# Performance work log

Hardware: AMD Instinct MI355X
Metric: run time of the kernel (lower is better)

## Reference

```python
import jax, jax.numpy as jnp
import numpy as np


def setup_inputs() -> dict:
    key = jax.random.key(0)
    k1, k2, k3, k4, k5 = jax.random.split(key, 5)
    C, Cr = 512, 64  # in_channels, in_channels // 8
    B, W, H = 16, 64, 64
    x = jax.random.normal(k1, (B, C, W, H), dtype=jnp.float32)
    # 1x1 conv == pointwise linear over channels; store as [out, in]
    w1 = jax.random.normal(k2, (Cr, C), dtype=jnp.float32) * (1.0 / np.sqrt(C))
    b1 = jax.random.normal(k3, (Cr,), dtype=jnp.float32) * 0.01
    w2 = jax.random.normal(k4, (C, Cr), dtype=jnp.float32) * (1.0 / np.sqrt(Cr))
    b2 = jax.random.normal(k5, (C,), dtype=jnp.float32) * 0.01
    return {"x": x, "w1": w1, "b1": b1, "w2": w2, "b2": b2}


def reference(x, w1, b1, w2, b2):
    B, C, W, H = x.shape
    # conv1x1: channel reduction C -> C//8
    r = jnp.einsum('bchw,oc->bohw', x, w1) + b1[None, :, None, None]
    q = r.reshape(B, -1, W * H)                      # [B, C', N] query/key/value
    # channel-channel attention map [B, C', C'] (bmm(query, key^T))
    att = jnp.einsum('bcn,bdn->bcd', q, q)
    att = jax.nn.softmax(att, axis=-1)
    out = jnp.einsum('bcd,bdn->bcn', att, q)          # [B, C', N]
    out = out.reshape(B, -1, W, H)
    # conv_out: channel expansion C//8 -> C, plus residual
    out = jnp.einsum('bchw,oc->bohw', out, w2) + b2[None, :, None, None]
    return out + x
```

## Files before the change

kernel.cpp:

```cpp
#include <hip/hip_runtime.h>
#include <math.h>

#define NPIX 4096
#define CIN  512
#define CR   64
#define NB   16

typedef __bf16 bf16x8 __attribute__((ext_vector_type(8)));
typedef float  f32x4  __attribute__((ext_vector_type(4)));
typedef unsigned int uint;
typedef uint   uint4v __attribute__((ext_vector_type(4)));
typedef unsigned short ushort;

static const size_t W1B_OFF = 0;
static const size_t Q_OFF   = W1B_OFF + 65536;
static const size_t QT_OFF  = Q_OFF  + (size_t)NB*CR*NPIX*2;
static const size_t ATT_OFF = QT_OFF + (size_t)NB*NPIX*CR*2;
static const size_t MB_OFF  = ATT_OFF + (size_t)NB*CR*CR*4;

static __device__ inline uint pk_bf16(float a, float b) {
    uint r;
    asm volatile("v_cvt_pk_bf16_f32 %0, %1, %2" : "=v"(r) : "v"(a), "v"(b));
    return r;
}

__global__ __launch_bounds__(256) void k0_cast(const float* __restrict__ w1,
                                               uint* __restrict__ w1b) {
    int i = blockIdx.x * 256 + threadIdx.x;
    w1b[i] = pk_bf16(w1[2 * i], w1[2 * i + 1]);
}

__global__ __launch_bounds__(256) void k1_conv1(const float* __restrict__ x,
                                                const ushort* __restrict__ w1b,
                                                const float* __restrict__ b1,
                                                ushort* __restrict__ q,
                                                ushort* __restrict__ qt) {
    int b = blockIdx.y;
    int t = threadIdx.x;
    int wid = t >> 6, l = t & 63;
    int lo = l & 15, kg = l >> 4;
    int px0 = blockIdx.x * 256 + wid * 64;
    const float* xb = x + (size_t)b * CIN * NPIX;

    f32x4 acc[4][4] = {};
    for (int ks = 0; ks < 16; ks++) {
        int k0 = ks * 32 + kg * 8;
        float xv[4][8];
#pragma unroll
        for (int pf = 0; pf < 4; pf++) {
            const float* xp = xb + (size_t)k0 * NPIX + px0 + pf * 16 + lo;
#pragma unroll
            for (int j = 0; j < 8; j++) xv[pf][j] = xp[(size_t)j * NPIX];
        }
        bf16x8 af[4];
#pragma unroll
        for (int of = 0; of < 4; of++)
            af[of] = *(const bf16x8*)(w1b + (size_t)(of * 16 + lo) * CIN + k0);
#pragma unroll
        for (int pf = 0; pf < 4; pf++) {
            uint4v bu;
#pragma unroll
            for (int j = 0; j < 4; j++) bu[j] = pk_bf16(xv[pf][2 * j], xv[pf][2 * j + 1]);
            bf16x8 bf = __builtin_bit_cast(bf16x8, bu);
#pragma unroll
            for (int of = 0; of < 4; of++)
                acc[pf][of] = __builtin_amdgcn_mfma_f32_16x16x32_bf16(af[of], bf, acc[pf][of], 0, 0, 0);
        }
    }
#pragma unroll
    for (int pf = 0; pf < 4; pf++) {
        int px = px0 + pf * 16 + lo;
        ushort* qb  = q  + (size_t)b * CR * NPIX + px;
        ushort* qtb = qt + ((size_t)b * NPIX + px) * CR;
#pragma unroll
        for (int of = 0; of < 4; of++) {
            int o = of * 16 + kg * 4;
            float v0 = acc[pf][of][0] + b1[o + 0];
            float v1 = acc[pf][of][1] + b1[o + 1];
            float v2 = acc[pf][of][2] + b1[o + 2];
            float v3 = acc[pf][of][3] + b1[o + 3];
            uint p0 = pk_bf16(v0, v1), p1 = pk_bf16(v2, v3);
            qb[(size_t)(o + 0) * NPIX] = (ushort)(p0 & 0xffff);
            qb[(size_t)(o + 1) * NPIX] = (ushort)(p0 >> 16);
            qb[(size_t)(o + 2) * NPIX] = (ushort)(p1 & 0xffff);
            qb[(size_t)(o + 3) * NPIX] = (ushort)(p1 >> 16);
            *(uint2*)(qtb + o) = make_uint2(p0, p1);
        }
    }
}

__global__ __launch_bounds__(512) void k2_att(const ushort* __restrict__ q,
                                              float* __restrict__ att) {
    __shared__ float part[8][64][66];
    int b = blockIdx.x;
    int t = threadIdx.x;
    int w = t >> 6, l = t & 63;
    int lo = l & 15, kg = l >> 4;
    const ushort* qb = q + (size_t)b * CR * NPIX + w * 512;

    f32x4 acc[4][4] = {};
    for (int ks = 0; ks < 16; ks++) {
        bf16x8 fr[4];
#pragma unroll
        for (int cf = 0; cf < 4; cf++)
            fr[cf] = *(const bf16x8*)(qb + (size_t)(cf * 16 + lo) * NPIX + ks * 32 + kg * 8);
#pragma unroll
        for (int cf = 0; cf < 4; cf++)
#pragma unroll
            for (int df = 0; df < 4; df++)
                acc[cf][df] = __builtin_amdgcn_mfma_f32_16x16x32_bf16(fr[cf], fr[df], acc[cf][df], 0, 0, 0);
    }
#pragma unroll
    for (int cf = 0; cf < 4; cf++)
#pragma unroll
        for (int df = 0; df < 4; df++)
#pragma unroll
            for (int r = 0; r < 4; r++)
                part[w][cf * 16 + kg * 4 + r][df * 16 + lo] = acc[cf][df][r];
    __syncthreads();

#pragma unroll
    for (int i = 0; i < 8; i++) {
        int c = w * 8 + i;
        float v = 0.f;
#pragma unroll
        for (int pw = 0; pw < 8; pw++) v += part[pw][c][l];
        float m = v;
#pragma unroll
        for (int s = 1; s < 64; s <<= 1) m = fmaxf(m, __shfl_xor(m, s, 64));
        float e = __expf(v - m);
        float ssum = e;
#pragma unroll
        for (int s = 1; s < 64; s <<= 1) ssum += __shfl_xor(ssum, s, 64);
        att[((size_t)b * CR + c) * CR + l] = e / ssum;
    }
}

__global__ __launch_bounds__(256) void k3_m(const float* __restrict__ w2,
                                            const float* __restrict__ att,
                                            ushort* __restrict__ mb) {
    int b = blockIdx.y;
    int c  = (blockIdx.x >> 2) * 256 + threadIdx.x;
    int dg = (blockIdx.x & 3) * 16;
    const float* ab  = att + (size_t)b * CR * CR + dg;
    const float* w2r = w2 + (size_t)c * CR;
    float acc[16];
#pragma unroll
    for (int j = 0; j < 16; j++) acc[j] = 0.f;
    for (int k = 0; k < CR; k++) {
        float wv = w2r[k];
#pragma unroll
        for (int j4 = 0; j4 < 4; j4++) {
            f32x4 av = *(const f32x4*)(ab + k * CR + j4 * 4);
#pragma unroll
            for (int u = 0; u < 4; u++)
                acc[j4 * 4 + u] = fmaf(wv, av[u], acc[j4 * 4 + u]);
        }
    }
    uint* mp = (uint*)(mb + ((size_t)b * CIN + c) * CR + dg);
#pragma unroll
    for (int i = 0; i < 8; i++)
        mp[i] = pk_bf16(acc[2 * i], acc[2 * i + 1]);
}

__global__ __launch_bounds__(256) void k4_out(const ushort* __restrict__ qt,
                                              const ushort* __restrict__ mb,
                                              const float* __restrict__ b2,
                                              const float* __restrict__ x,
                                              float* __restrict__ y) {
    int cc = blockIdx.x, b = blockIdx.z;
    int t = threadIdx.x;
    int wid = t >> 6, l = t & 63;
    int lo = l & 15, kg = l >> 4;
    int px0 = blockIdx.y * 128 + wid * 32;
    int pxA = px0 + lo, pxB = px0 + 16 + lo;
    const ushort* qpA = qt + ((size_t)b * NPIX + pxA) * CR;
    const ushort* qpB = qt + ((size_t)b * NPIX + pxB) * CR;
    const ushort* mp = mb + ((size_t)b * CIN + cc * 64) * CR;

    bf16x8 bqA0 = *(const bf16x8*)(qpA + kg * 8);
    bf16x8 bqA1 = *(const bf16x8*)(qpA + 32 + kg * 8);
    bf16x8 bqB0 = *(const bf16x8*)(qpB + kg * 8);
    bf16x8 bqB1 = *(const bf16x8*)(qpB + 32 + kg * 8);
    bf16x8 am[4][2];
#pragma unroll
    for (int cf = 0; cf < 4; cf++) {
        am[cf][0] = *(const bf16x8*)(mp + (size_t)(cf * 16 + lo) * CR + kg * 8);
        am[cf][1] = *(const bf16x8*)(mp + (size_t)(cf * 16 + lo) * CR + 32 + kg * 8);
    }
    float xrA[4][4], xrB[4][4];
#pragma unroll
    for (int cf = 0; cf < 4; cf++)
#pragma unroll
        for (int r = 0; r < 4; r++) {
            size_t row = ((size_t)b * CIN + cc * 64 + cf * 16 + kg * 4 + r) * NPIX;
            xrA[cf][r] = x[row + pxA];
            xrB[cf][r] = x[row + pxB];
        }

    f32x4 accA[4] = {}, accB[4] = {};
#pragma unroll
    for (int cf = 0; cf < 4; cf++) {
        accA[cf] = __builtin_amdgcn_mfma_f32_16x16x32_bf16(am[cf][0], bqA0, accA[cf], 0, 0, 0);
        accA[cf] = __builtin_amdgcn_mfma_f32_16x16x32_bf16(am[cf][1], bqA1, accA[cf], 0, 0, 0);
        accB[cf] = __builtin_amdgcn_mfma_f32_16x16x32_bf16(am[cf][0], bqB0, accB[cf], 0, 0, 0);
        accB[cf] = __builtin_amdgcn_mfma_f32_16x16x32_bf16(am[cf][1], bqB1, accB[cf], 0, 0, 0);
    }
#pragma unroll
    for (int cf = 0; cf < 4; cf++) {
        int c = cc * 64 + cf * 16 + kg * 4;
#pragma unroll
        for (int r = 0; r < 4; r++) {
            size_t row = ((size_t)b * CIN + c + r) * NPIX;
            y[row + pxA] = accA[cf][r] + b2[c + r] + xrA[cf][r];
            y[row + pxB] = accB[cf][r] + b2[c + r] + xrB[cf][r];
        }
    }
}

extern "C" void kernel_launch(void* const* d_in, const int* in_sizes, int n_in,
                              void* d_out, int out_size, void* d_ws, size_t ws_size,
                              hipStream_t stream) {
    const float* x  = (const float*)d_in[0];
    const float* w1 = (const float*)d_in[1];
    const float* b1 = (const float*)d_in[2];
    const float* w2 = (const float*)d_in[3];
    const float* b2 = (const float*)d_in[4];
    float* y = (float*)d_out;
    char* ws = (char*)d_ws;

    uint*   w1b = (uint*)  (ws + W1B_OFF);
    ushort* q   = (ushort*)(ws + Q_OFF);
    ushort* qt  = (ushort*)(ws + QT_OFF);
    float*  att = (float*) (ws + ATT_OFF);
    ushort* mb  = (ushort*)(ws + MB_OFF);

    hipLaunchKernelGGL(k0_cast,  dim3(64),         dim3(256), 0, stream, w1, w1b);
    hipLaunchKernelGGL(k1_conv1, dim3(16, 16),     dim3(256), 0, stream, x, (const ushort*)w1b, b1, q, qt);
    hipLaunchKernelGGL(k2_att,   dim3(16),         dim3(512), 0, stream, q, att);
    hipLaunchKernelGGL(k3_m,     dim3(8, 16),      dim3(256), 0, stream, w2, att, mb);
    hipLaunchKernelGGL(k4_out,   dim3(8, 32, 16),  dim3(256), 0, stream, qt, mb, b2, x, y);
}
```

Measured before the change: 118.5 us.

## Double-buffer conv1 loads, tile qt for coalesced stores, widen att block

The conv1 kernel now double-buffers its x and weight loads across K-steps, so global loads for the next step are issued while MFMAs run on the current one. The transposed q buffer is re-laid out in MFMA-fragment-tiled order, making both the conv1 stores and the output-kernel loads contiguous across lanes. The attention kernel uses 1024 threads (16 waves), each reducing half as many pixels, with a two-phase shared-memory accumulation. The cost is higher register pressure in conv1 and an extra sync in the attention kernel.

```diff
diff --git a/kernel.cpp b/kernel.cpp
--- a/kernel.cpp
+++ b/kernel.cpp
@@ -18,6 +18,7 @@
 static const size_t ATT_OFF = QT_OFF + (size_t)NB*NPIX*CR*2;
 static const size_t MB_OFF  = ATT_OFF + (size_t)NB*CR*CR*4;
 
+
 static __device__ inline uint pk_bf16(float a, float b) {
     uint r;
     asm volatile("v_cvt_pk_bf16_f32 %0, %1, %2" : "=v"(r) : "v"(a), "v"(b));
@@ -30,48 +31,64 @@
     w1b[i] = pk_bf16(w1[2 * i], w1[2 * i + 1]);
 }
 
+#define K1_LOAD(XV, AF, KS) do {                                             \
+    int k0_ = (KS) * 32 + kg * 8;                                            \
+    _Pragma("unroll")                                                        \
+    for (int pf = 0; pf < 4; pf++) {                                         \
+        const float* xp_ = xb + (size_t)k0_ * NPIX + pf * 16;                \
+        _Pragma("unroll")                                                    \
+        for (int j = 0; j < 8; j++) XV[pf][j] = xp_[(size_t)j * NPIX];       \
+    }                                                                        \
+    _Pragma("unroll")                                                        \
+    for (int of = 0; of < 4; of++)                                           \
+        AF[of] = *(const bf16x8*)(w1b + (size_t)(of * 16 + lo) * CIN + k0_); \
+} while (0)
+
+#define K1_COMPUTE(XV, AF) do {                                              \
+    _Pragma("unroll")                                                        \
+    for (int pf = 0; pf < 4; pf++) {                                         \
+        uint4v bu_;                                                          \
+        _Pragma("unroll")                                                    \
+        for (int j = 0; j < 4; j++)                                          \
+            bu_[j] = pk_bf16(XV[pf][2 * j], XV[pf][2 * j + 1]);              \
+        bf16x8 bf_ = __builtin_bit_cast(bf16x8, bu_);                        \
+        _Pragma("unroll")                                                    \
+        for (int of = 0; of < 4; of++)                                       \
+            acc[pf][of] = __builtin_amdgcn_mfma_f32_16x16x32_bf16(           \
+                AF[of], bf_, acc[pf][of], 0, 0, 0);                          \
+    }                                                                        \
+} while (0)
+
 __global__ __launch_bounds__(256) void k1_conv1(const float* __restrict__ x,
                                                 const ushort* __restrict__ w1b,
                                                 const float* __restrict__ b1,
                                                 ushort* __restrict__ q,
-                                                ushort* __restrict__ qt) {
+                                                uint2* __restrict__ qt4) {
     int b = blockIdx.y;
     int t = threadIdx.x;
     int wid = t >> 6, l = t & 63;
     int lo = l & 15, kg = l >> 4;
     int px0 = blockIdx.x * 256 + wid * 64;
-    const float* xb = x + (size_t)b * CIN * NPIX;
+    const float* xb = x + (size_t)b * CIN * NPIX + px0 + lo;
 
     f32x4 acc[4][4] = {};
-    for (int ks = 0; ks < 16; ks++) {
-        int k0 = ks * 32 + kg * 8;
-        float xv[4][8];
-#pragma unroll
-        for (int pf = 0; pf < 4; pf++) {
-            const float* xp = xb + (size_t)k0 * NPIX + px0 + pf * 16 + lo;
-#pragma unroll
-            for (int j = 0; j < 8; j++) xv[pf][j] = xp[(size_t)j * NPIX];
-        }
-        bf16x8 af[4];
-#pragma unroll
-        for (int of = 0; of < 4; of++)
-            af[of] = *(const bf16x8*)(w1b + (size_t)(of * 16 + lo) * CIN + k0);
-#pragma unroll
-        for (int pf = 0; pf < 4; pf++) {
-            uint4v bu;
-#pragma unroll
-            for (int j = 0; j < 4; j++) bu[j] = pk_bf16(xv[pf][2 * j], xv[pf][2 * j + 1]);
-            bf16x8 bf = __builtin_bit_cast(bf16x8, bu);
-#pragma unroll
-            for (int of = 0; of < 4; of++)
-                acc[pf][of] = __builtin_amdgcn_mfma_f32_16x16x32_bf16(af[of], bf, acc[pf][of], 0, 0, 0);
-        }
-    }
+    float xvA[4][8], xvB[4][8];
+    bf16x8 afA[4], afB[4];
+
+    K1_LOAD(xvA, afA, 0);
+#pragma unroll
+    for (int ks2 = 0; ks2 < 8; ks2++) {
+        K1_LOAD(xvB, afB, 2 * ks2 + 1);
+        K1_COMPUTE(xvA, afA);
+        if (ks2 < 7) K1_LOAD(xvA, afA, 2 * ks2 + 2);
+        K1_COMPUTE(xvB, afB);
+    }
+
 #pragma unroll
     for (int pf = 0; pf < 4; pf++) {
         int px = px0 + pf * 16 + lo;
-        ushort* qb  = q  + (size_t)b * CR * NPIX + px;
-        ushort* qtb = qt + ((size_t)b * NPIX + px) * CR;
+        ushort* qb = q + (size_t)b * CR * NPIX + px;
+        uint2* qt4b = qt4 + (((size_t)b * 256 + (px0 >> 4) + pf) * 4) * 64 + kg * 16 + lo;
 #pragma unroll
         for (int of = 0; of < 4; of++) {
             int o = of * 16 + kg * 4;
@@ -84,22 +101,23 @@
             qb[(size_t)(o + 1) * NPIX] = (ushort)(p0 >> 16);
             qb[(size_t)(o + 2) * NPIX] = (ushort)(p1 & 0xffff);
             qb[(size_t)(o + 3) * NPIX] = (ushort)(p1 >> 16);
-            *(uint2*)(qtb + o) = make_uint2(p0, p1);
-        }
-    }
-}
-
-__global__ __launch_bounds__(512) void k2_att(const ushort* __restrict__ q,
-                                              float* __restrict__ att) {
+            qt4b[of * 64] = make_uint2(p0, p1);
+        }
+    }
+}
+
+__global__ __launch_bounds__(1024) void k2_att(const ushort* __restrict__ q,
+                                               float* __restrict__ att) {
     __shared__ float part[8][64][66];
     int b = blockIdx.x;
     int t = threadIdx.x;
     int w = t >> 6, l = t & 63;
     int lo = l & 15, kg = l >> 4;
-    const ushort* qb = q + (size_t)b * CR * NPIX + w * 512;
+    const ushort* qb = q + (size_t)b * CR * NPIX + w * 256;
 
     f32x4 acc[4][4] = {};
-    for (int ks = 0; ks < 16; ks++) {
+#pragma unroll 2
+    for (int ks = 0; ks < 8; ks++) {
         bf16x8 fr[4];
 #pragma unroll
         for (int cf = 0; cf < 4; cf++)
@@ -110,18 +128,31 @@
             for (int df = 0; df < 4; df++)
                 acc[cf][df] = __builtin_amdgcn_mfma_f32_16x16x32_bf16(fr[cf], fr[df], acc[cf][df], 0, 0, 0);
     }
-#pragma unroll
-    for (int cf = 0; cf < 4; cf++)
-#pragma unroll
-        for (int df = 0; df < 4; df++)
-#pragma unroll
-            for (int r = 0; r < 4; r++)
-                part[w][cf * 16 + kg * 4 + r][df * 16 + lo] = acc[cf][df][r];
+    if (w < 8) {
+#pragma unroll
+        for (int cf = 0; cf < 4; cf++)
+#pragma unroll
+            for (int df = 0; df < 4; df++)
+#pragma unroll
+                for (int r = 0; r < 4; r++)
+                    part[w][cf * 16 + kg * 4 + r][df * 16 + lo] = acc[cf][df][r];
+    }
     __syncthreads();
-
-#pragma unroll
-    for (int i = 0; i < 8; i++) {
-        int c = w * 8 + i;
+    if (w >= 8) {
+        int ws = w - 8;
+#pragma unroll
+        for (int cf = 0; cf < 4; cf++)
+#pragma unroll
+            for (int df = 0; df < 4; df++)
+#pragma unroll
+                for (int r = 0; r < 4; r++)
+                    part[ws][cf * 16 + kg * 4 + r][df * 16 + lo] += acc[cf][df][r];
+    }
+    __syncthreads();
+
+#pragma unroll
+    for (int i = 0; i < 4; i++) {
+        int c = w * 4 + i;
         float v = 0.f;
 #pragma unroll
         for (int pw = 0; pw < 8; pw++) v += part[pw][c][l];
@@ -163,7 +194,7 @@
         mp[i] = pk_bf16(acc[2 * i], acc[2 * i + 1]);
 }
 
-__global__ __launch_bounds__(256) void k4_out(const ushort* __restrict__ qt,
+__global__ __launch_bounds__(256) void k4_out(const uint2* __restrict__ qt4,
                                               const ushort* __restrict__ mb,
                                               const float* __restrict__ b2,
                                               const float* __restrict__ x,
@@ -174,14 +205,21 @@
     int lo = l & 15, kg = l >> 4;
     int px0 = blockIdx.y * 128 + wid * 32;
     int pxA = px0 + lo, pxB = px0 + 16 + lo;
-    const ushort* qpA = qt + ((size_t)b * NPIX + pxA) * CR;
-    const ushort* qpB = qt + ((size_t)b * NPIX + pxB) * CR;
+    const uint2* qt4b = qt4 + (size_t)b * 65536;
     const ushort* mp = mb + ((size_t)b * CIN + cc * 64) * CR;
 
-    bf16x8 bqA0 = *(const bf16x8*)(qpA + kg * 8);
-    bf16x8 bqA1 = *(const bf16x8*)(qpA + 32 + kg * 8);
-    bf16x8 bqB0 = *(const bf16x8*)(qpB + kg * 8);
-    bf16x8 bqB1 = *(const bf16x8*)(qpB + 32 + kg * 8);
+#define QT4_LD(PXHI, PXLO, M)                                                  \
+    ({ int of_ = (M) >> 1, kgA_ = ((M) & 1) * 2;                               \
+       const uint2* p_ = qt4b + (((size_t)(PXHI) * 4 + of_) * 4 + kgA_) * 16 + (PXLO); \
+       uint2 g0_ = p_[0], g1_ = p_[16];                                        \
+       uint4v u_; u_[0] = g0_.x; u_[1] = g0_.y; u_[2] = g1_.x; u_[3] = g1_.y;  \
+       __builtin_bit_cast(bf16x8, u_); })
+
+    int pxhi = px0 >> 4;
+    bf16x8 bqA0 = QT4_LD(pxhi,     lo, kg);
+    bf16x8 bqA1 = QT4_LD(pxhi,     lo, 4 + kg);
+    bf16x8 bqB0 = QT4_LD(pxhi + 1, lo, kg);
+    bf16x8 bqB1 = QT4_LD(pxhi + 1, lo, 4 + kg);
     bf16x8 am[4][2];
 #pragma unroll
     for (int cf = 0; cf < 4; cf++) {
@@ -231,13 +269,13 @@
 
     uint*   w1b = (uint*)  (ws + W1B_OFF);
     ushort* q   = (ushort*)(ws + Q_OFF);
-    ushort* qt  = (ushort*)(ws + QT_OFF);
+    uint2*  qt4 = (uint2*) (ws + QT_OFF);
     float*  att = (float*) (ws + ATT_OFF);
     ushort* mb  = (ushort*)(ws + MB_OFF);
 
-    hipLaunchKernelGGL(k0_cast,  dim3(64),         dim3(256), 0, stream, w1, w1b);
-    hipLaunchKernelGGL(k1_conv1, dim3(16, 16),     dim3(256), 0, stream, x, (const ushort*)w1b, b1, q, qt);
-    hipLaunchKernelGGL(k2_att,   dim3(16),         dim3(512), 0, stream, q, att);
-    hipLaunchKernelGGL(k3_m,     dim3(8, 16),      dim3(256), 0, stream, w2, att, mb);
-    hipLaunchKernelGGL(k4_out,   dim3(8, 32, 16),  dim3(256), 0, stream, qt, mb, b2, x, y);
-}
+    hipLaunchKernelGGL(k0_cast,  dim3(64),         dim3(256),  0, stream, w1, w1b);
+    hipLaunchKernelGGL(k1_conv1, dim3(16, 16),     dim3(256),  0, stream, x, (const ushort*)w1b, b1, q, qt4);
+    hipLaunchKernelGGL(k2_att,   dim3(16),         dim3(1024), 0, stream, q, att);
+    hipLaunchKernelGGL(k3_m,     dim3(8, 16),      dim3(256),  0, stream, w2, att, mb);
+    hipLaunchKernelGGL(k4_out,   dim3(8, 32, 16),  dim3(256),  0, stream, qt4, mb, b2, x, y);
+}
```

Measured after the change: 116.4 us. About the same (-1.8%).
